# Kernel tuning notes

Measured on AMD Instinct MI355X. Metric: run time of the kernel, lower is better.

The kernel has to match this reference:

```python
import jax, jax.numpy as jnp
import numpy as np

N_NODES = 50000


def gcn_conv(x, W, b, src, dst, n_nodes):
    # Linear transform first (PyG GCNConv): [N, out]
    h = x @ W
    # Add self-loops
    loop = jnp.arange(n_nodes, dtype=src.dtype)
    s = jnp.concatenate([src, loop])
    d = jnp.concatenate([dst, loop])
    # Symmetric normalization: deg counted at destination with unit weights
    deg = jax.ops.segment_sum(jnp.ones_like(d, dtype=h.dtype), d, num_segments=n_nodes)
    dinv = jnp.where(deg > 0, jax.lax.rsqrt(deg), 0.0)
    norm = dinv[s] * dinv[d]  # [E+N]
    # Gather source features, scale, scatter-add to destinations
    msgs = h[s] * norm[:, None]
    out = jax.ops.segment_sum(msgs, d, num_segments=n_nodes)
    return out + b


def setup_inputs() -> dict:
    key = jax.random.key(0)
    k1, k2, k3, k4, k5 = jax.random.split(key, 5)
    in_c, out_c = 512, 128
    x = jax.random.normal(k1, (N_NODES, in_c), dtype=jnp.float32)
    edge_index = jax.random.randint(k2, (2, 800000), 0, N_NODES, dtype=jnp.int64)
    glorot = 1.0 / np.sqrt(in_c)
    W_mu = jax.random.uniform(k3, (in_c, out_c), jnp.float32, -glorot, glorot)
    W_logstd = jax.random.uniform(k4, (in_c, out_c), jnp.float32, -glorot, glorot)
    b_mu = jnp.zeros((out_c,), jnp.float32)
    b_logstd = jnp.zeros((out_c,), jnp.float32)
    return {"x": x, "edge_index": edge_index, "W_mu": W_mu, "b_mu": b_mu,
            "W_logstd": W_logstd, "b_logstd": b_logstd}


def reference(x, edge_index, W_mu, b_mu, W_logstd, b_logstd):
    src, dst = edge_index[0], edge_index[1]
    mu = gcn_conv(x, W_mu, b_mu, src, dst, N_NODES)
    logstd = gcn_conv(x, W_logstd, b_logstd, src, dst, N_NODES)
    return mu, logstd
```

## Files before the change

### kernel.cpp

```cpp
#include <hip/hip_runtime.h>

#define NN 50000
#define NE 800000
#define KC 512
#define OC 256
#define NB_SCAN 196

typedef float f32x4 __attribute__((ext_vector_type(4)));
typedef short bf16x8 __attribute__((ext_vector_type(8)));

__device__ __forceinline__ unsigned f2bf(float f) {
    union { float f; unsigned u; } v; v.f = f;
    return (v.u + 0x7FFFu + ((v.u >> 16) & 1u)) >> 16;
}
__device__ __forceinline__ float bf2f(unsigned short b) {
    union { unsigned u; float f; } v; v.u = ((unsigned)b) << 16;
    return v.f;
}

__global__ __launch_bounds__(256) void count_deg_kernel(const int* __restrict__ ei,
                                                        int* __restrict__ deg) {
    int e = blockIdx.x * 256 + threadIdx.x;
    if (e < NE) atomicAdd(&deg[ei[NE + e]], 1);
}

__global__ __launch_bounds__(256) void scan_part_kernel(const int* __restrict__ deg,
                                                        int* __restrict__ partial) {
    int tid = threadIdx.x;
    int i = blockIdx.x * 256 + tid;
    int v = (i < NN) ? deg[i] : 0;
#pragma unroll
    for (int off = 32; off > 0; off >>= 1) v += __shfl_down(v, off, 64);
    __shared__ int wsum[4];
    if ((tid & 63) == 0) wsum[tid >> 6] = v;
    __syncthreads();
    if (tid == 0) partial[blockIdx.x] = wsum[0] + wsum[1] + wsum[2] + wsum[3];
}

__global__ __launch_bounds__(256) void scan_block_kernel(const int* __restrict__ partial,
                                                         int* __restrict__ blockoff) {
    __shared__ int lds[256];
    int tid = threadIdx.x;
    int v = (tid < NB_SCAN) ? partial[tid] : 0;
    lds[tid] = v;
    __syncthreads();
    for (int off = 1; off < 256; off <<= 1) {
        int t = (tid >= off) ? lds[tid - off] : 0;
        __syncthreads();
        lds[tid] += t;
        __syncthreads();
    }
    if (tid < NB_SCAN) blockoff[tid] = lds[tid] - v;
}

__global__ __launch_bounds__(256) void scan_apply_kernel(const int* __restrict__ deg,
                                                         const int* __restrict__ blockoff,
                                                         int* __restrict__ row_start,
                                                         int* __restrict__ cursor,
                                                         float* __restrict__ dinv) {
    int tid = threadIdx.x;
    int lane = tid & 63;
    int w = tid >> 6;
    int i = blockIdx.x * 256 + tid;
    int d = (i < NN) ? deg[i] : 0;
    int v = d;
#pragma unroll
    for (int off = 1; off < 64; off <<= 1) {
        int t = __shfl_up(v, off, 64);
        if (lane >= off) v += t;
    }
    __shared__ int wsum[4];
    if (lane == 63) wsum[w] = v;
    __syncthreads();
    int wof = 0;
    for (int k = 0; k < w; ++k) wof += wsum[k];
    int excl = blockoff[blockIdx.x] + wof + v - d;
    if (i < NN) {
        row_start[i] = excl;
        cursor[i] = excl;
        dinv[i] = rsqrtf((float)(d + 1));
    }
    if (i == NN - 1) row_start[NN] = excl + d;
}

__global__ __launch_bounds__(256) void scatter_kernel(const int* __restrict__ ei,
                                                      int* __restrict__ cursor,
                                                      int* __restrict__ csr_src) {
    int e = blockIdx.x * 256 + threadIdx.x;
    if (e < NE) {
        int d = ei[NE + e];
        int pos = atomicAdd(&cursor[d], 1);
        csr_src[pos] = ei[e];
    }
}

__global__ __launch_bounds__(256) void convw_kernel(const float* __restrict__ Wmu,
                                                    const float* __restrict__ Wls,
                                                    uint4* __restrict__ Wc) {
    int idx = blockIdx.x * 256 + threadIdx.x;
    int kb = idx >> 10;
    int rem = idx & 1023;
    int wf = rem >> 6;
    int lane = rem & 63;
    int g4 = lane >> 4;
    int i16 = lane & 15;
    int col = (wf >> 2) * 64 + (wf & 3) * 16 + i16;
    int k0 = kb * 32 + g4 * 8;
    const float* Wsrc = (col < 128) ? (Wmu + col) : (Wls + (col - 128));
    unsigned o[4];
#pragma unroll
    for (int p = 0; p < 4; ++p) {
        float lo = Wsrc[(size_t)(k0 + 2 * p) * 128];
        float hi = Wsrc[(size_t)(k0 + 2 * p + 1) * 128];
        o[p] = f2bf(lo) | (f2bf(hi) << 16);
    }
    uint4 v;
    v.x = o[0]; v.y = o[1]; v.z = o[2]; v.w = o[3];
    Wc[idx] = v;
}

#define ALD 136
__global__ __launch_bounds__(256, 4) void gemm_kernel(const float* __restrict__ x,
                                                      const uint4* __restrict__ Wc,
                                                      const float* __restrict__ dinv,
                                                      unsigned short* __restrict__ hs) {
    __shared__ __align__(16) unsigned short As[2][32 * ALD];

    int tid = threadIdx.x;
    int lane = tid & 63;
    int w = tid >> 6;
    int r0 = blockIdx.x * 32;
    int i16 = lane & 15;
    int g4 = lane >> 4;

    int st_row = tid >> 3;
    int st_c = tid & 7;
    int xr = r0 + st_row;
    if (xr > NN - 1) xr = NN - 1;
    const float* xg = x + (size_t)xr * KC + st_c * 16;
    unsigned short* adst = &As[0][st_row * ALD + st_c * 16];

    float4 xa[2][4];
    auto loadA = [&](int set, int S) {
#pragma unroll
        for (int i = 0; i < 4; ++i) xa[set][i] = *(const float4*)(xg + S * 128 + i * 4);
    };
    auto storeA = [&](int buf, int set) {
        uint4* dst = (uint4*)(adst + buf * 32 * ALD);
#pragma unroll
        for (int p = 0; p < 2; ++p) {
            uint4 o;
            o.x = f2bf(xa[set][2 * p].x) | (f2bf(xa[set][2 * p].y) << 16);
            o.y = f2bf(xa[set][2 * p].z) | (f2bf(xa[set][2 * p].w) << 16);
            o.z = f2bf(xa[set][2 * p + 1].x) | (f2bf(xa[set][2 * p + 1].y) << 16);
            o.w = f2bf(xa[set][2 * p + 1].z) | (f2bf(xa[set][2 * p + 1].w) << 16);
            dst[p] = o;
        }
    };

    const uint4* wbase = Wc + (size_t)(w * 4) * 64 + lane;
    uint4 bb[2][4];
    auto loadB = [&](int dbuf, int kb) {
#pragma unroll
        for (int fc = 0; fc < 4; ++fc) bb[dbuf][fc] = wbase[kb * 1024 + fc * 64];
    };

    f32x4 acc[2][4];
    f32x4 zz = {0.f, 0.f, 0.f, 0.f};
#pragma unroll
    for (int a = 0; a < 2; ++a)
#pragma unroll
        for (int b = 0; b < 4; ++b) acc[a][b] = zz;

    loadA(0, 0);
    storeA(0, 0);
    __syncthreads();
    loadA(1, 1);
    loadA(0, 2);
    loadB(0, 0);

#pragma unroll
    for (int S = 0; S < 4; ++S) {
#pragma unroll
        for (int ks = 0; ks < 4; ++ks) {
            const int kb = S * 4 + ks;
            const int cur = kb & 1;
            if (kb < 15) loadB(cur ^ 1, kb + 1);
            bf16x8 af[2];
#pragma unroll
            for (int fr = 0; fr < 2; ++fr)
                af[fr] = *(const bf16x8*)&As[S & 1][(fr * 16 + i16) * ALD + ks * 32 + g4 * 8];
#pragma unroll
            for (int fc = 0; fc < 4; ++fc) {
                bf16x8 bfrag = *(const bf16x8*)&bb[cur][fc];
#pragma unroll
                for (int fr = 0; fr < 2; ++fr)
                    acc[fr][fc] = __builtin_amdgcn_mfma_f32_16x16x32_bf16(af[fr], bfrag, acc[fr][fc], 0, 0, 0);
            }
        }
        if (S < 3) {
            storeA((S + 1) & 1, (S + 1) & 1);
            __syncthreads();
            if (S == 0) loadA(1, 3);
        }
    }

#pragma unroll
    for (int fr = 0; fr < 2; ++fr) {
#pragma unroll
        for (int r = 0; r < 4; ++r) {
            int gr = r0 + fr * 16 + g4 * 4 + r;
            if (gr < NN) {
                float dv = dinv[gr];
#pragma unroll
                for (int fc = 0; fc < 4; ++fc) {
                    int col = w * 64 + fc * 16 + i16;
                    hs[(size_t)gr * OC + col] = (unsigned short)f2bf(acc[fr][fc][r] * dv);
                }
            }
        }
    }
}

__global__ __launch_bounds__(256) void aggregate_kernel(const unsigned short* __restrict__ hs,
                                                        const int* __restrict__ row_start,
                                                        const int* __restrict__ csr_src,
                                                        const float* __restrict__ dinv,
                                                        const float* __restrict__ bmu,
                                                        const float* __restrict__ bls,
                                                        float* __restrict__ out) {
    int tid = threadIdx.x;
    int lane = tid & 63;
    int node = blockIdx.x * 4 + (tid >> 6);

    const unsigned short* hrow = hs + lane * 4;
    float acc0, acc1, acc2, acc3;
    {
        ushort4 v = *(const ushort4*)&hrow[(size_t)node * OC];
        acc0 = bf2f(v.x);
        acc1 = bf2f(v.y);
        acc2 = bf2f(v.z);
        acc3 = bf2f(v.w);
    }
    int rs = row_start[node], re = row_start[node + 1];
    int e = rs;
    for (; e + 8 <= re; e += 8) {
        int s[8];
#pragma unroll
        for (int q = 0; q < 8; ++q) s[q] = csr_src[e + q];
        ushort4 v[8];
#pragma unroll
        for (int q = 0; q < 8; ++q) v[q] = *(const ushort4*)&hrow[(size_t)s[q] * OC];
#pragma unroll
        for (int q = 0; q < 8; ++q) {
            acc0 += bf2f(v[q].x);
            acc1 += bf2f(v[q].y);
            acc2 += bf2f(v[q].z);
            acc3 += bf2f(v[q].w);
        }
    }
    if (e + 4 <= re) {
        int s[4];
#pragma unroll
        for (int q = 0; q < 4; ++q) s[q] = csr_src[e + q];
        ushort4 v[4];
#pragma unroll
        for (int q = 0; q < 4; ++q) v[q] = *(const ushort4*)&hrow[(size_t)s[q] * OC];
#pragma unroll
        for (int q = 0; q < 4; ++q) {
            acc0 += bf2f(v[q].x);
            acc1 += bf2f(v[q].y);
            acc2 += bf2f(v[q].z);
            acc3 += bf2f(v[q].w);
        }
        e += 4;
    }
    for (; e < re; ++e) {
        int s0 = csr_src[e];
        ushort4 v0 = *(const ushort4*)&hrow[(size_t)s0 * OC];
        acc0 += bf2f(v0.x);
        acc1 += bf2f(v0.y);
        acc2 += bf2f(v0.z);
        acc3 += bf2f(v0.w);
    }
    float dn = dinv[node];
    if (lane < 32) {
        f32x4 b = *(const f32x4*)&bmu[lane * 4];
        f32x4 r;
        r.x = acc0 * dn + b.x;
        r.y = acc1 * dn + b.y;
        r.z = acc2 * dn + b.z;
        r.w = acc3 * dn + b.w;
        __builtin_nontemporal_store(r, (f32x4*)(out + (size_t)node * 128 + lane * 4));
    } else {
        f32x4 b = *(const f32x4*)&bls[(lane - 32) * 4];
        f32x4 r;
        r.x = acc0 * dn + b.x;
        r.y = acc1 * dn + b.y;
        r.z = acc2 * dn + b.z;
        r.w = acc3 * dn + b.w;
        __builtin_nontemporal_store(
            r, (f32x4*)(out + (size_t)NN * 128 + (size_t)node * 128 + (lane - 32) * 4));
    }
}

extern "C" void kernel_launch(void* const* d_in, const int* in_sizes, int n_in,
                              void* d_out, int out_size, void* d_ws, size_t ws_size,
                              hipStream_t stream) {
    const float* x = (const float*)d_in[0];
    const int* ei = (const int*)d_in[1];
    const float* Wmu = (const float*)d_in[2];
    const float* bmu = (const float*)d_in[3];
    const float* Wls = (const float*)d_in[4];
    const float* bls = (const float*)d_in[5];
    float* out = (float*)d_out;

    char* ws = (char*)d_ws;
    size_t off = 0;
    auto alloc = [&](size_t bytes) {
        void* p = ws + off;
        off += (bytes + 255) & ~(size_t)255;
        return p;
    };
    unsigned short* hs = (unsigned short*)alloc((size_t)NN * OC * sizeof(unsigned short));
    uint4* Wc = (uint4*)alloc((size_t)16384 * 16);
    int* deg = (int*)alloc((size_t)NN * sizeof(int));
    int* row_start = (int*)alloc((size_t)(NN + 1) * sizeof(int));
    int* cursor = (int*)alloc((size_t)NN * sizeof(int));
    int* csr_src = (int*)alloc((size_t)NE * sizeof(int));
    float* dinv = (float*)alloc((size_t)NN * sizeof(float));
    int* partial = (int*)alloc((size_t)NB_SCAN * sizeof(int));
    int* blockoff = (int*)alloc((size_t)NB_SCAN * sizeof(int));

    hipMemsetAsync(deg, 0, (size_t)NN * sizeof(int), stream);

    count_deg_kernel<<<(NE + 255) / 256, 256, 0, stream>>>(ei, deg);
    scan_part_kernel<<<NB_SCAN, 256, 0, stream>>>(deg, partial);
    scan_block_kernel<<<1, 256, 0, stream>>>(partial, blockoff);
    scan_apply_kernel<<<NB_SCAN, 256, 0, stream>>>(deg, blockoff, row_start, cursor, dinv);
    scatter_kernel<<<(NE + 255) / 256, 256, 0, stream>>>(ei, cursor, csr_src);
    convw_kernel<<<64, 256, 0, stream>>>(Wmu, Wls, Wc);
    gemm_kernel<<<(NN + 31) / 32, 256, 0, stream>>>(x, Wc, dinv, hs);
    aggregate_kernel<<<NN / 4, 256, 0, stream>>>(hs, row_start, csr_src, dinv, bmu, bls, out);
}
```

Measured before the change: 199.3 us.

## Stream x tiles directly into LDS via global_load_lds and convert at read

The GEMM's A operand (fp32 x) is now copied straight from global memory into an XOR-swizzled fp32 LDS buffer with global_load_lds, instead of going through registers and a software bf16 conversion. Conversion to bf16 moves to the LDS read side using the hardware v_cvt_pk_bf16_f32 instruction. The W fragment prefetch deepens from double to triple buffering. The aim is to cut register pressure and VALU conversion work and to overlap the x loads with MFMA. In exchange the fp32 tile doubles LDS use per block, which may limit occupancy, and each x element is converted once per reading wave rather than once per tile.

After: 196.9 us. Within noise of the previous version (-1.2%).

```diff
diff --git a/kernel.cpp b/kernel.cpp
--- a/kernel.cpp
+++ b/kernel.cpp
@@ -119,12 +119,11 @@
     Wc[idx] = v;
 }
 
-#define ALD 136
 __global__ __launch_bounds__(256, 4) void gemm_kernel(const float* __restrict__ x,
                                                       const uint4* __restrict__ Wc,
                                                       const float* __restrict__ dinv,
                                                       unsigned short* __restrict__ hs) {
-    __shared__ __align__(16) unsigned short As[2][32 * ALD];
+    __shared__ __align__(16) float Af[2][32 * 128];
 
     int tid = threadIdx.x;
     int lane = tid & 63;
@@ -133,33 +132,47 @@
     int i16 = lane & 15;
     int g4 = lane >> 4;
 
-    int st_row = tid >> 3;
-    int st_c = tid & 7;
-    int xr = r0 + st_row;
-    if (xr > NN - 1) xr = NN - 1;
-    const float* xg = x + (size_t)xr * KC + st_c * 16;
-    unsigned short* adst = &As[0][st_row * ALD + st_c * 16];
-
-    float4 xa[2][4];
-    auto loadA = [&](int set, int S) {
-#pragma unroll
-        for (int i = 0; i < 4; ++i) xa[set][i] = *(const float4*)(xg + S * 128 + i * 4);
+    const float* srcp[4];
+#pragma unroll
+    for (int j = 0; j < 4; ++j) {
+        int r = w * 8 + j * 2 + (lane >> 5);
+        int gr = r0 + r;
+        if (gr > NN - 1) gr = NN - 1;
+        int cp = (lane & 31) >> 1;
+        int mp = (lane & 1) * 4;
+        int c = cp ^ (r & 15);
+        int m = mp ^ (((r >> 2) & 1) * 4);
+        srcp[j] = x + (size_t)gr * KC + c * 8 + m;
+    }
+    auto dmaA = [&](int buf, int S) {
+#pragma unroll
+        for (int j = 0; j < 4; ++j) {
+            __builtin_amdgcn_global_load_lds(
+                (const __attribute__((address_space(1))) void*)(srcp[j] + S * 128),
+                (__attribute__((address_space(3))) void*)&Af[buf][(w * 4 + j) * 256], 16, 0, 0);
+        }
     };
-    auto storeA = [&](int buf, int set) {
-        uint4* dst = (uint4*)(adst + buf * 32 * ALD);
-#pragma unroll
-        for (int p = 0; p < 2; ++p) {
-            uint4 o;
-            o.x = f2bf(xa[set][2 * p].x) | (f2bf(xa[set][2 * p].y) << 16);
-            o.y = f2bf(xa[set][2 * p].z) | (f2bf(xa[set][2 * p].w) << 16);
-            o.z = f2bf(xa[set][2 * p + 1].x) | (f2bf(xa[set][2 * p + 1].y) << 16);
-            o.w = f2bf(xa[set][2 * p + 1].z) | (f2bf(xa[set][2 * p + 1].w) << 16);
-            dst[p] = o;
-        }
+
+    auto readA = [&](int buf, int ks, int fr) -> bf16x8 {
+        int r = fr * 16 + i16;
+        int c = ks * 4 + g4;
+        int cc = c ^ (r & 15);
+        int mo = ((r >> 2) & 1) * 4;
+        const float* p = &Af[buf][r * 128 + cc * 8];
+        f32x4 lo = *(const f32x4*)(p + mo);
+        f32x4 hi = *(const f32x4*)(p + (mo ^ 4));
+        unsigned o0, o1, o2, o3;
+        asm("v_cvt_pk_bf16_f32 %0, %1, %2" : "=v"(o0) : "v"(lo.x), "v"(lo.y));
+        asm("v_cvt_pk_bf16_f32 %0, %1, %2" : "=v"(o1) : "v"(lo.z), "v"(lo.w));
+        asm("v_cvt_pk_bf16_f32 %0, %1, %2" : "=v"(o2) : "v"(hi.x), "v"(hi.y));
+        asm("v_cvt_pk_bf16_f32 %0, %1, %2" : "=v"(o3) : "v"(hi.z), "v"(hi.w));
+        union { unsigned u[4]; bf16x8 v; } res;
+        res.u[0] = o0; res.u[1] = o1; res.u[2] = o2; res.u[3] = o3;
+        return res.v;
     };
 
     const uint4* wbase = Wc + (size_t)(w * 4) * 64 + lane;
-    uint4 bb[2][4];
+    uint4 bb[3][4];
     auto loadB = [&](int dbuf, int kb) {
 #pragma unroll
         for (int fc = 0; fc < 4; ++fc) bb[dbuf][fc] = wbase[kb * 1024 + fc * 64];
@@ -172,37 +185,29 @@
 #pragma unroll
         for (int b = 0; b < 4; ++b) acc[a][b] = zz;
 
-    loadA(0, 0);
-    storeA(0, 0);
+    dmaA(0, 0);
+    loadB(0, 0);
+    loadB(1, 1);
     __syncthreads();
-    loadA(1, 1);
-    loadA(0, 2);
-    loadB(0, 0);
 
 #pragma unroll
     for (int S = 0; S < 4; ++S) {
+        if (S < 3) dmaA((S + 1) & 1, S + 1);
 #pragma unroll
         for (int ks = 0; ks < 4; ++ks) {
             const int kb = S * 4 + ks;
-            const int cur = kb & 1;
-            if (kb < 15) loadB(cur ^ 1, kb + 1);
-            bf16x8 af[2];
-#pragma unroll
-            for (int fr = 0; fr < 2; ++fr)
-                af[fr] = *(const bf16x8*)&As[S & 1][(fr * 16 + i16) * ALD + ks * 32 + g4 * 8];
+            if (kb + 2 < 16) loadB((kb + 2) % 3, kb + 2);
+            bf16x8 af0 = readA(S & 1, ks, 0);
+            bf16x8 af1 = readA(S & 1, ks, 1);
+            const int cur = kb % 3;
 #pragma unroll
             for (int fc = 0; fc < 4; ++fc) {
                 bf16x8 bfrag = *(const bf16x8*)&bb[cur][fc];
-#pragma unroll
-                for (int fr = 0; fr < 2; ++fr)
-                    acc[fr][fc] = __builtin_amdgcn_mfma_f32_16x16x32_bf16(af[fr], bfrag, acc[fr][fc], 0, 0, 0);
+                acc[0][fc] = __builtin_amdgcn_mfma_f32_16x16x32_bf16(af0, bfrag, acc[0][fc], 0, 0, 0);
+                acc[1][fc] = __builtin_amdgcn_mfma_f32_16x16x32_bf16(af1, bfrag, acc[1][fc], 0, 0, 0);
             }
         }
-        if (S < 3) {
-            storeA((S + 1) & 1, (S + 1) & 1);
-            __syncthreads();
-            if (S == 0) loadA(1, 3);
-        }
+        if (S < 3) __syncthreads();
     }
 
 #pragma unroll
```
